# Optimization experiments

Hardware: AMD Instinct MI355X
Metric: run time of the kernel (lower is better)

Reference implementation:

```python
import jax, jax.numpy as jnp
import numpy as np

D = 1024
H = 16
DH = D // H
SCALE = DH ** -0.5
EPS = 1e-5


def setup_inputs() -> dict:
    key = jax.random.key(0)
    ks = jax.random.split(key, 8)
    B, K = 256, 64
    hidden = jax.random.normal(ks[0], (B, K, D), dtype=jnp.float32)
    active_mask = jax.random.bernoulli(ks[1], 0.5, (B, K))
    w = lambda k: jax.random.normal(k, (D, D), dtype=jnp.float32) * 0.02
    return {
        "hidden": hidden,
        "active_mask": active_mask,
        "W_q": w(ks[2]),
        "W_k": w(ks[3]),
        "W_v": w(ks[4]),
        "W_o": w(ks[5]),
        "ln_gamma": jnp.ones((D,), dtype=jnp.float32),
        "ln_beta": jnp.zeros((D,), dtype=jnp.float32),
    }


def reference(hidden, active_mask, W_q, W_k, W_v, W_o, ln_gamma, ln_beta):
    B, K, _ = hidden.shape
    # Linear (no bias): x @ W.T, then split heads -> [B, H, K, Dh]
    def heads(t):
        return t.reshape(B, K, H, DH).transpose(0, 2, 1, 3)
    Q = heads(hidden @ W_q.T)
    Km = heads(hidden @ W_k.T)
    V = heads(hidden @ W_v.T)
    # scaled dot-product scores [B, H, K, K]
    attn = jnp.einsum("bhqd,bhkd->bhqk", Q, Km) * SCALE
    attn = jax.nn.softmax(attn, axis=-1)
    # post-softmax row masking: inactive query rows get zero attention
    row_mask = active_mask[:, None, :, None].astype(attn.dtype)  # [B,1,K,1]
    attn = attn * row_mask
    out = jnp.einsum("bhqk,bhkd->bhqd", attn, V)
    out = out.transpose(0, 2, 1, 3).reshape(B, K, D)
    out = out @ W_o.T
    # gated residual: residual attention output only on active modules
    active_f = active_mask[:, :, None].astype(hidden.dtype)
    h_final = hidden + active_f * out
    # LayerNorm over last dim
    mu = jnp.mean(h_final, axis=-1, keepdims=True)
    var = jnp.var(h_final, axis=-1, keepdims=True)
    h_norm = (h_final - mu) * jax.lax.rsqrt(var + EPS)
    return h_norm * ln_gamma + ln_beta
```

## Files before the change

### kernel.cpp

```cpp
#include <hip/hip_runtime.h>
#include <hip/hip_bf16.h>
#include <stdint.h>

#define D_DIM 1024
#define NH 16
#define DHD 64
#define SEQ 64
#define NBATCH 256
#define M_TOT 16384
#define ATT_SCALE 0.125f
#define LN_EPS 1e-5f

#define BM 256
#define BN 256
#define BKT 64
#define NTK (D_DIM / BKT)

typedef __attribute__((ext_vector_type(8))) short bf16x8;
typedef __attribute__((ext_vector_type(4))) float f32x4;

__device__ __forceinline__ float bf2f(short s) {
  union { uint32_t u; float f; } c;
  c.u = ((uint32_t)(uint16_t)s) << 16;
  return c.f;
}

__device__ __forceinline__ short f2bf(float f) {
  union { __hip_bfloat16 h; short s; } c; c.h = __float2bfloat16(f);
  return c.s;
}

__device__ __forceinline__ bf16x8 cvt8(float4 a, float4 b) {
  bf16x8 r;
  r[0] = f2bf(a.x); r[1] = f2bf(a.y); r[2] = f2bf(a.z); r[3] = f2bf(a.w);
  r[4] = f2bf(b.x); r[5] = f2bf(b.y); r[6] = f2bf(b.z); r[7] = f2bf(b.w);
  return r;
}

__device__ __forceinline__ void cp16(const void* g, void* l) {
  __builtin_amdgcn_global_load_lds(
      (const __attribute__((address_space(1))) uint32_t*)g,
      (__attribute__((address_space(3))) uint32_t*)l, 16, 0, 0);
}

__global__ void conv_all(const float* __restrict__ Wq, const float* __restrict__ Wk,
                         const float* __restrict__ Wv, const float* __restrict__ Wo,
                         const float* __restrict__ H,
                         __hip_bfloat16* __restrict__ Wall,
                         __hip_bfloat16* __restrict__ Hb) {
  const size_t idx8 = ((size_t)blockIdx.x * 256 + threadIdx.x) * 8;
  const size_t WE = (size_t)4 * D_DIM * D_DIM;
  const float* src;
  __hip_bfloat16* dst;
  if (idx8 < WE) {
    int z = (int)(idx8 >> 20);
    size_t off = idx8 & ((1u << 20) - 1);
    src = ((z == 0) ? Wq : (z == 1) ? Wk : (z == 2) ? Wv : Wo) + off;
    dst = Wall + idx8;
  } else {
    size_t off = idx8 - WE;
    src = H + off;
    dst = Hb + off;
  }
  float4 a = ((const float4*)src)[0];
  float4 b = ((const float4*)src)[1];
  *(bf16x8*)(short*)dst = cvt8(a, b);
}

#define GEMM_TILE(J, CUR, NXT) do {                                           \
    _Pragma("unroll") for (int i_ = 0; i_ < 4; ++i_) {                        \
      af[i_][0] = *(const bf16x8*)(LdsA[CUR] + aoff + i_ * 2048 + colsw0);    \
      af[i_][1] = *(const bf16x8*)(LdsA[CUR] + aoff + i_ * 2048 + colsw1);    \
    }                                                                         \
    _Pragma("unroll") for (int q_ = 0; q_ < 2; ++q_) {                        \
      bfr[q_][0] = *(const bf16x8*)(LdsB[CUR] + boff + q_ * 2048 + colsw0);   \
      bfr[q_][1] = *(const bf16x8*)(LdsB[CUR] + boff + q_ * 2048 + colsw1);   \
    }                                                                         \
    __builtin_amdgcn_s_barrier();                                             \
    __asm volatile("s_waitcnt lgkmcnt(0)" ::: "memory");                      \
    __builtin_amdgcn_s_setprio(1);                                            \
    _Pragma("unroll") for (int i_ = 0; i_ < 4; ++i_)                          \
      _Pragma("unroll") for (int q_ = 0; q_ < 2; ++q_) {                      \
        acc[i_][q_] = __builtin_amdgcn_mfma_f32_16x16x32_bf16(                \
            af[i_][0], bfr[q_][0], acc[i_][q_], 0, 0, 0);                     \
        acc[i_][q_] = __builtin_amdgcn_mfma_f32_16x16x32_bf16(                \
            af[i_][1], bfr[q_][1], acc[i_][q_], 0, 0, 0);                     \
      }                                                                       \
    __builtin_amdgcn_s_setprio(0);                                            \
    __builtin_amdgcn_s_barrier();                                             \
    _Pragma("unroll") for (int q_ = 0; q_ < 2; ++q_) {                        \
      bfr[2 + q_][0] =                                                        \
          *(const bf16x8*)(LdsB[CUR] + boff + (2 + q_) * 2048 + colsw0);      \
      bfr[2 + q_][1] =                                                        \
          *(const bf16x8*)(LdsB[CUR] + boff + (2 + q_) * 2048 + colsw1);      \
    }                                                                         \
    if ((J) + 2 < NTK) { STG_A(CUR, (J) + 2, 0); STG_A(CUR, (J) + 2, 2); }    \
    __builtin_amdgcn_s_barrier();                                             \
    __asm volatile("s_waitcnt lgkmcnt(0)" ::: "memory");                      \
    __builtin_amdgcn_s_setprio(1);                                            \
    _Pragma("unroll") for (int i_ = 0; i_ < 4; ++i_)                          \
      _Pragma("unroll") for (int q_ = 0; q_ < 2; ++q_) {                      \
        acc[i_][2 + q_] = __builtin_amdgcn_mfma_f32_16x16x32_bf16(            \
            af[i_][0], bfr[2 + q_][0], acc[i_][2 + q_], 0, 0, 0);             \
        acc[i_][2 + q_] = __builtin_amdgcn_mfma_f32_16x16x32_bf16(            \
            af[i_][1], bfr[2 + q_][1], acc[i_][2 + q_], 0, 0, 0);             \
      }                                                                       \
    __builtin_amdgcn_s_setprio(0);                                            \
    __builtin_amdgcn_s_barrier();                                             \
    _Pragma("unroll") for (int i_ = 0; i_ < 4; ++i_) {                        \
      af[i_][0] =                                                             \
          *(const bf16x8*)(LdsA[CUR] + aoff + 8192 + i_ * 2048 + colsw0);     \
      af[i_][1] =                                                             \
          *(const bf16x8*)(LdsA[CUR] + aoff + 8192 + i_ * 2048 + colsw1);     \
    }                                                                         \
    if ((J) + 2 < NTK) {                                                      \
      STG_B(CUR, (J) + 2, 0); STG_B(CUR, (J) + 2, 1);                         \
      STG_B(CUR, (J) + 2, 2); STG_B(CUR, (J) + 2, 3);                         \
    }                                                                         \
    __builtin_amdgcn_s_barrier();                                             \
    __asm volatile("s_waitcnt lgkmcnt(0)" ::: "memory");                      \
    __builtin_amdgcn_s_setprio(1);                                            \
    _Pragma("unroll") for (int i_ = 0; i_ < 4; ++i_)                          \
      _Pragma("unroll") for (int q_ = 0; q_ < 2; ++q_) {                      \
        acc[4 + i_][2 + q_] = __builtin_amdgcn_mfma_f32_16x16x32_bf16(        \
            af[i_][0], bfr[2 + q_][0], acc[4 + i_][2 + q_], 0, 0, 0);         \
        acc[4 + i_][2 + q_] = __builtin_amdgcn_mfma_f32_16x16x32_bf16(        \
            af[i_][1], bfr[2 + q_][1], acc[4 + i_][2 + q_], 0, 0, 0);         \
      }                                                                       \
    __builtin_amdgcn_s_setprio(0);                                            \
    __builtin_amdgcn_s_barrier();                                             \
    if ((J) + 2 < NTK) { STG_A(CUR, (J) + 2, 1); STG_A(CUR, (J) + 2, 3); }    \
    __builtin_amdgcn_s_setprio(1);                                            \
    _Pragma("unroll") for (int i_ = 0; i_ < 4; ++i_)                          \
      _Pragma("unroll") for (int q_ = 0; q_ < 2; ++q_) {                      \
        acc[4 + i_][q_] = __builtin_amdgcn_mfma_f32_16x16x32_bf16(            \
            af[i_][0], bfr[q_][0], acc[4 + i_][q_], 0, 0, 0);                 \
        acc[4 + i_][q_] = __builtin_amdgcn_mfma_f32_16x16x32_bf16(            \
            af[i_][1], bfr[q_][1], acc[4 + i_][q_], 0, 0, 0);                 \
      }                                                                       \
    __builtin_amdgcn_s_setprio(0);                                            \
    if ((J) + 2 < NTK) {                                                      \
      __asm volatile("s_waitcnt vmcnt(8)" ::: "memory");                      \
    } else if ((J) + 1 < NTK) {                                               \
      __asm volatile("s_waitcnt vmcnt(0)" ::: "memory");                      \
    }                                                                         \
    __builtin_amdgcn_s_barrier();                                             \
  } while (0)

#define GEMM_PIPELINE() do {                                                  \
    STG_A(0, 0, 0); STG_A(0, 0, 1); STG_A(0, 0, 2); STG_A(0, 0, 3);           \
    STG_B(0, 0, 0); STG_B(0, 0, 1); STG_B(0, 0, 2); STG_B(0, 0, 3);           \
    STG_A(1, 1, 0); STG_A(1, 1, 1); STG_A(1, 1, 2); STG_A(1, 1, 3);           \
    STG_B(1, 1, 0); STG_B(1, 1, 1); STG_B(1, 1, 2); STG_B(1, 1, 3);           \
    __asm volatile("s_waitcnt vmcnt(8)" ::: "memory");                        \
    __builtin_amdgcn_s_barrier();                                             \
    _Pragma("unroll 1") for (int it_ = 0; it_ < NTK / 2; ++it_) {             \
      GEMM_TILE(2 * it_, 0, 1);                                               \
      GEMM_TILE(2 * it_ + 1, 1, 0);                                           \
    }                                                                         \
  } while (0)

__global__ void __launch_bounds__(512, 2)
gemm_qkv_bf(const __hip_bfloat16* __restrict__ Hb,
            const __hip_bfloat16* __restrict__ Wall,
            __hip_bfloat16* __restrict__ Qw,
            __hip_bfloat16* __restrict__ Kw,
            __hip_bfloat16* __restrict__ Vtw) {
  __shared__ __align__(16) char LdsA[2][BM * BKT * 2];
  __shared__ __align__(16) char LdsB[2][BN * BKT * 2];
  const int tid = threadIdx.x;
  const int lane = tid & 63, wave = tid >> 6;
  const int l16 = lane & 15, kq = lane >> 4;
  const int wr = wave >> 2, wc = wave & 3;
  const int m0 = blockIdx.x * BM, n0 = blockIdx.y * BN;
  const __hip_bfloat16* Bm = Wall + (size_t)blockIdx.z * D_DIM * D_DIM;
  const int wub = wave * 1024;
  const int srow = tid >> 3;
  const int scol8 = (((tid >> 3) & 7) ^ (tid & 7)) << 3;
  const size_t a_thr = (size_t)(m0 + srow) * D_DIM + scol8;
  const size_t b_thr = (size_t)(n0 + srow) * D_DIM + scol8;
  const int colsw0 = (kq * 16) ^ ((l16 & 7) << 4);
  const int colsw1 = (64 + kq * 16) ^ ((l16 & 7) << 4);
  const int aoff = (wr * 128 + l16) * 128;
  const int boff = (wc * 64 + l16) * 128;

  f32x4 acc[8][4] = {};
  bf16x8 af[4][2], bfr[4][2];

#define STG_A(BUF, JT, Q)                                                      \
  cp16(Hb + a_thr + (size_t)(Q) * (64 * D_DIM) + (JT) * BKT,                   \
       LdsA[BUF] + (Q) * 8192 + wub)
#define STG_B(BUF, JT, Q)                                                      \
  cp16(Bm + b_thr + (size_t)(Q) * (64 * D_DIM) + (JT) * BKT,                   \
       LdsB[BUF] + (Q) * 8192 + wub)

  GEMM_PIPELINE();

#undef STG_A
#undef STG_B

  __hip_bfloat16* outp = (blockIdx.z == 0) ? Qw : (blockIdx.z == 1) ? Kw : Vtw;
  const int zlt2 = (blockIdx.z < 2);
#pragma unroll
  for (int i = 0; i < 8; ++i) {
#pragma unroll
    for (int r = 0; r < 4; ++r) {
      int gm = m0 + wr * 128 + i * 16 + kq * 4 + r;
      int b = gm >> 6, ks = gm & 63;
#pragma unroll
      for (int jf = 0; jf < 4; ++jf) {
        int gn = n0 + wc * 64 + jf * 16 + l16;
        int h = gn >> 6, dh = gn & 63;
        size_t idx = zlt2 ? ((size_t)(b * NH + h) * SEQ + ks) * DHD + dh
                          : ((size_t)(b * NH + h) * DHD + dh) * SEQ + ks;
        outp[idx] = __float2bfloat16(acc[i][jf][r]);
      }
    }
  }
}

__global__ void attn_v2(__hip_bfloat16* Qw,
                        const __hip_bfloat16* __restrict__ Kw,
                        const __hip_bfloat16* __restrict__ Vtw,
                        const int* __restrict__ mask) {
  __shared__ __align__(16) __hip_bfloat16 Ps[4][16 * 72];
  const int tid = threadIdx.x;
  const int lane = tid & 63;
  const int wave = tid >> 6;
  const int l16 = lane & 15, kq = lane >> 4;
  const int hh = blockIdx.x * 4 + wave;
  const int b = hh >> 4;
  const size_t base = (size_t)hh * 4096;
  __hip_bfloat16* Pw = &Ps[wave][0];

  bf16x8 kf[2][4], vf[2][4], qf[4][2];
#pragma unroll
  for (int kk2 = 0; kk2 < 2; ++kk2)
#pragma unroll
    for (int j = 0; j < 4; ++j) {
      kf[kk2][j] = *(const bf16x8*)(Kw + base + (j * 16 + l16) * 64 + kk2 * 32 + kq * 8);
      vf[kk2][j] = *(const bf16x8*)(Vtw + base + (j * 16 + l16) * 64 + kk2 * 32 + kq * 8);
    }
#pragma unroll
  for (int qt = 0; qt < 4; ++qt)
#pragma unroll
    for (int kk2 = 0; kk2 < 2; ++kk2)
      qf[qt][kk2] = *(const bf16x8*)(Qw + base + (qt * 16 + l16) * 64 + kk2 * 32 + kq * 8);

#pragma unroll
  for (int qt = 0; qt < 4; ++qt) {
    f32x4 accS[4] = {};
#pragma unroll
    for (int kk2 = 0; kk2 < 2; ++kk2)
#pragma unroll
      for (int j = 0; j < 4; ++j)
        accS[j] = __builtin_amdgcn_mfma_f32_16x16x32_bf16(qf[qt][kk2], kf[kk2][j],
                                                          accS[j], 0, 0, 0);
#pragma unroll
    for (int r = 0; r < 4; ++r) {
      float sv[4];
      float m = -1e30f;
#pragma unroll
      for (int j = 0; j < 4; ++j) { sv[j] = accS[j][r] * ATT_SCALE; m = fmaxf(m, sv[j]); }
#pragma unroll
      for (int off = 1; off < 16; off <<= 1) m = fmaxf(m, __shfl_xor(m, off, 64));
      float s = 0.f;
#pragma unroll
      for (int j = 0; j < 4; ++j) { sv[j] = __expf(sv[j] - m); s += sv[j]; }
#pragma unroll
      for (int off = 1; off < 16; off <<= 1) s += __shfl_xor(s, off, 64);
      float inv = 1.0f / s;
      int ql = kq * 4 + r;
#pragma unroll
      for (int j = 0; j < 4; ++j)
        Pw[ql * 72 + j * 16 + l16] = __float2bfloat16(sv[j] * inv);
    }
    __asm volatile("s_waitcnt lgkmcnt(0)" ::: "memory");

    f32x4 accO[4] = {};
#pragma unroll
    for (int kk2 = 0; kk2 < 2; ++kk2) {
      bf16x8 a = *(const bf16x8*)((const short*)Pw + l16 * 72 + kk2 * 32 + kq * 8);
#pragma unroll
      for (int j = 0; j < 4; ++j)
        accO[j] = __builtin_amdgcn_mfma_f32_16x16x32_bf16(a, vf[kk2][j], accO[j], 0, 0, 0);
    }
    __asm volatile("s_waitcnt lgkmcnt(0)" ::: "memory");

#pragma unroll
    for (int r = 0; r < 4; ++r) {
      int q = qt * 16 + kq * 4 + r;
      float mk = mask[b * SEQ + q] ? 1.0f : 0.0f;
#pragma unroll
      for (int j = 0; j < 4; ++j)
        Qw[base + q * DHD + j * 16 + l16] = __float2bfloat16(accO[j][r] * mk);
    }
  }
}

__global__ void __launch_bounds__(512, 2)
gemm_o(const __hip_bfloat16* __restrict__ Ow,
       const __hip_bfloat16* __restrict__ WoB,
       const int* __restrict__ mask,
       __hip_bfloat16* Hb) {
  __shared__ __align__(16) char LdsA[2][BM * BKT * 2];
  __shared__ __align__(16) char LdsB[2][BN * BKT * 2];
  const int tid = threadIdx.x;
  const int lane = tid & 63, wave = tid >> 6;
  const int l16 = lane & 15, kq = lane >> 4;
  const int wr = wave >> 2, wc = wave & 3;
  const int m0 = blockIdx.x * BM, n0 = blockIdx.y * BN;
  const int wub = wave * 1024;
  const int srow = tid >> 3;
  const int scol8 = (((tid >> 3) & 7) ^ (tid & 7)) << 3;
  const size_t ao_thr = ((size_t)(m0 >> 6) << 16) + (srow << 6) + scol8;
  const size_t b_thr = (size_t)(n0 + srow) * D_DIM + scol8;
  const int colsw0 = (kq * 16) ^ ((l16 & 7) << 4);
  const int colsw1 = (64 + kq * 16) ^ ((l16 & 7) << 4);
  const int aoff = (wr * 128 + l16) * 128;
  const int boff = (wc * 64 + l16) * 128;

  f32x4 acc[8][4] = {};
  bf16x8 af[4][2], bfr[4][2];

#define STG_A(BUF, JT, Q)                                                      \
  cp16(Ow + ao_thr + ((size_t)(Q) << 16) + ((size_t)(JT) << 12),               \
       LdsA[BUF] + (Q) * 8192 + wub)
#define STG_B(BUF, JT, Q)                                                      \
  cp16(WoB + b_thr + (size_t)(Q) * (64 * D_DIM) + (JT) * BKT,                  \
       LdsB[BUF] + (Q) * 8192 + wub)

  GEMM_PIPELINE();

#undef STG_A
#undef STG_B

#pragma unroll
  for (int i = 0; i < 8; ++i) {
#pragma unroll
    for (int r = 0; r < 4; ++r) {
      int gm = m0 + wr * 128 + i * 16 + kq * 4 + r;
      float mk = mask[gm] ? 1.0f : 0.0f;
#pragma unroll
      for (int jf = 0; jf < 4; ++jf) {
        int gn = n0 + wc * 64 + jf * 16 + l16;
        size_t idx = (size_t)gm * D_DIM + gn;
        Hb[idx] = __float2bfloat16(__bfloat162float(Hb[idx]) + mk * acc[i][jf][r]);
      }
    }
  }
}

__global__ void __launch_bounds__(512)
ln_bf(const __hip_bfloat16* __restrict__ Hf,
      const float* __restrict__ gamma,
      const float* __restrict__ beta,
      float* __restrict__ out) {
  const int tid = threadIdx.x;
  const int wave = tid >> 6, lane = tid & 63;
  const int row = blockIdx.x * 8 + wave;
  const size_t rb = (size_t)row * D_DIM + lane * 16;

  bf16x8 v0 = *(const bf16x8*)((const short*)Hf + rb);
  bf16x8 v1 = *(const bf16x8*)((const short*)Hf + rb + 8);
  float f[16], s = 0.f, ss = 0.f;
#pragma unroll
  for (int k = 0; k < 8; ++k) { f[k] = bf2f(v0[k]); f[8 + k] = bf2f(v1[k]); }
#pragma unroll
  for (int k = 0; k < 16; ++k) { s += f[k]; ss += f[k] * f[k]; }
#pragma unroll
  for (int off = 1; off < 64; off <<= 1) {
    s += __shfl_xor(s, off, 64);
    ss += __shfl_xor(ss, off, 64);
  }
  const float mu = s * (1.0f / D_DIM);
  const float var = ss * (1.0f / D_DIM) - mu * mu;
  const float rs = rsqrtf(var + LN_EPS);

  const float4* gp = (const float4*)(gamma + lane * 16);
  const float4* bp = (const float4*)(beta + lane * 16);
  float4* op = (float4*)(out + rb);
#pragma unroll
  for (int q = 0; q < 4; ++q) {
    float4 g = gp[q], bb = bp[q];
    float4 o;
    o.x = (f[q * 4 + 0] - mu) * rs * g.x + bb.x;
    o.y = (f[q * 4 + 1] - mu) * rs * g.y + bb.y;
    o.z = (f[q * 4 + 2] - mu) * rs * g.z + bb.z;
    o.w = (f[q * 4 + 3] - mu) * rs * g.w + bb.w;
    op[q] = o;
  }
}

extern "C" void kernel_launch(void* const* d_in, const int* in_sizes, int n_in,
                              void* d_out, int out_size, void* d_ws, size_t ws_size,
                              hipStream_t stream) {
  const float* hidden = (const float*)d_in[0];
  const int* mask = (const int*)d_in[1];
  const float* Wq = (const float*)d_in[2];
  const float* Wk = (const float*)d_in[3];
  const float* Wv = (const float*)d_in[4];
  const float* Wo = (const float*)d_in[5];
  const float* gamma = (const float*)d_in[6];
  const float* beta = (const float*)d_in[7];
  float* out = (float*)d_out;

  const size_t SZ = (size_t)M_TOT * D_DIM;
  __hip_bfloat16* Hb   = (__hip_bfloat16*)d_ws;
  __hip_bfloat16* Kw   = Hb + SZ;
  __hip_bfloat16* Qw   = Hb + 2 * SZ;
  __hip_bfloat16* Vtw  = Hb + 3 * SZ;
  __hip_bfloat16* Wall = Hb + 4 * SZ;

  conv_all<<<dim3(10240), 256, 0, stream>>>(Wq, Wk, Wv, Wo, hidden, Wall, Hb);
  gemm_qkv_bf<<<dim3(64, 4, 3), 512, 0, stream>>>(Hb, Wall, Qw, Kw, Vtw);
  attn_v2<<<dim3(1024), 256, 0, stream>>>(Qw, Kw, Vtw, mask);
  gemm_o<<<dim3(64, 4), 512, 0, stream>>>(Qw, Wall + 3 * D_DIM * D_DIM, mask, Hb);
  ln_bf<<<dim3(2048), 512, 0, stream>>>(Hb, gamma, beta, out);
}
```

Before: 341.8 us.

## Shrink GEMM tiles to 128x128 with 4 waves and simplified pipeline

Both projection GEMMs move from 256x256 tiles with 8 waves to 128x128 tiles with 4 waves. The interleaved multi-phase MFMA/staging schedule becomes a single load-all-fragments-then-compute step per K tile. The aim is more blocks for better CU occupancy and load balance, since the old grids had only 256 or 768 blocks. In exchange, each block reuses loaded data less, global and LDS traffic per FLOP rises, and the loads no longer overlap the MFMAs within a tile.

Result: slower. 363.6 us (+6.4%).

```diff
diff --git a/kernel.cpp b/kernel.cpp
--- a/kernel.cpp
+++ b/kernel.cpp
@@ -11,8 +11,8 @@
 #define ATT_SCALE 0.125f
 #define LN_EPS 1e-5f
 
-#define BM 256
-#define BN 256
+#define BMS 128
+#define BNS 128
 #define BKT 64
 #define NTK (D_DIM / BKT)
 
@@ -67,79 +67,32 @@
   *(bf16x8*)(short*)dst = cvt8(a, b);
 }
 
-#define GEMM_TILE(J, CUR, NXT) do {                                           \
+#define GEMM_TILE_S(J, CUR, NXT) do {                                         \
     _Pragma("unroll") for (int i_ = 0; i_ < 4; ++i_) {                        \
       af[i_][0] = *(const bf16x8*)(LdsA[CUR] + aoff + i_ * 2048 + colsw0);    \
       af[i_][1] = *(const bf16x8*)(LdsA[CUR] + aoff + i_ * 2048 + colsw1);    \
     }                                                                         \
-    _Pragma("unroll") for (int q_ = 0; q_ < 2; ++q_) {                        \
-      bfr[q_][0] = *(const bf16x8*)(LdsB[CUR] + boff + q_ * 2048 + colsw0);   \
-      bfr[q_][1] = *(const bf16x8*)(LdsB[CUR] + boff + q_ * 2048 + colsw1);   \
+    _Pragma("unroll") for (int j_ = 0; j_ < 4; ++j_) {                        \
+      bfr[j_][0] = *(const bf16x8*)(LdsB[CUR] + boff + j_ * 2048 + colsw0);   \
+      bfr[j_][1] = *(const bf16x8*)(LdsB[CUR] + boff + j_ * 2048 + colsw1);   \
     }                                                                         \
-    __builtin_amdgcn_s_barrier();                                             \
-    __asm volatile("s_waitcnt lgkmcnt(0)" ::: "memory");                      \
     __builtin_amdgcn_s_setprio(1);                                            \
     _Pragma("unroll") for (int i_ = 0; i_ < 4; ++i_)                          \
-      _Pragma("unroll") for (int q_ = 0; q_ < 2; ++q_) {                      \
-        acc[i_][q_] = __builtin_amdgcn_mfma_f32_16x16x32_bf16(                \
-            af[i_][0], bfr[q_][0], acc[i_][q_], 0, 0, 0);                     \
-        acc[i_][q_] = __builtin_amdgcn_mfma_f32_16x16x32_bf16(                \
-            af[i_][1], bfr[q_][1], acc[i_][q_], 0, 0, 0);                     \
+      _Pragma("unroll") for (int j_ = 0; j_ < 4; ++j_) {                      \
+        acc[i_][j_] = __builtin_amdgcn_mfma_f32_16x16x32_bf16(                \
+            af[i_][0], bfr[j_][0], acc[i_][j_], 0, 0, 0);                     \
+        acc[i_][j_] = __builtin_amdgcn_mfma_f32_16x16x32_bf16(                \
+            af[i_][1], bfr[j_][1], acc[i_][j_], 0, 0, 0);                     \
       }                                                                       \
     __builtin_amdgcn_s_setprio(0);                                            \
+    __asm volatile("s_waitcnt lgkmcnt(0)" ::: "memory");                      \
+    __builtin_amdgcn_sched_barrier(0);                                        \
     __builtin_amdgcn_s_barrier();                                             \
-    _Pragma("unroll") for (int q_ = 0; q_ < 2; ++q_) {                        \
-      bfr[2 + q_][0] =                                                        \
-          *(const bf16x8*)(LdsB[CUR] + boff + (2 + q_) * 2048 + colsw0);      \
-      bfr[2 + q_][1] =                                                        \
-          *(const bf16x8*)(LdsB[CUR] + boff + (2 + q_) * 2048 + colsw1);      \
-    }                                                                         \
-    if ((J) + 2 < NTK) { STG_A(CUR, (J) + 2, 0); STG_A(CUR, (J) + 2, 2); }    \
-    __builtin_amdgcn_s_barrier();                                             \
-    __asm volatile("s_waitcnt lgkmcnt(0)" ::: "memory");                      \
-    __builtin_amdgcn_s_setprio(1);                                            \
-    _Pragma("unroll") for (int i_ = 0; i_ < 4; ++i_)                          \
-      _Pragma("unroll") for (int q_ = 0; q_ < 2; ++q_) {                      \
-        acc[i_][2 + q_] = __builtin_amdgcn_mfma_f32_16x16x32_bf16(            \
-            af[i_][0], bfr[2 + q_][0], acc[i_][2 + q_], 0, 0, 0);             \
-        acc[i_][2 + q_] = __builtin_amdgcn_mfma_f32_16x16x32_bf16(            \
-            af[i_][1], bfr[2 + q_][1], acc[i_][2 + q_], 0, 0, 0);             \
-      }                                                                       \
-    __builtin_amdgcn_s_setprio(0);                                            \
-    __builtin_amdgcn_s_barrier();                                             \
-    _Pragma("unroll") for (int i_ = 0; i_ < 4; ++i_) {                        \
-      af[i_][0] =                                                             \
-          *(const bf16x8*)(LdsA[CUR] + aoff + 8192 + i_ * 2048 + colsw0);     \
-      af[i_][1] =                                                             \
-          *(const bf16x8*)(LdsA[CUR] + aoff + 8192 + i_ * 2048 + colsw1);     \
-    }                                                                         \
     if ((J) + 2 < NTK) {                                                      \
+      STG_A(CUR, (J) + 2, 0); STG_A(CUR, (J) + 2, 1);                         \
+      STG_A(CUR, (J) + 2, 2); STG_A(CUR, (J) + 2, 3);                         \
       STG_B(CUR, (J) + 2, 0); STG_B(CUR, (J) + 2, 1);                         \
       STG_B(CUR, (J) + 2, 2); STG_B(CUR, (J) + 2, 3);                         \
-    }                                                                         \
-    __builtin_amdgcn_s_barrier();                                             \
-    __asm volatile("s_waitcnt lgkmcnt(0)" ::: "memory");                      \
-    __builtin_amdgcn_s_setprio(1);                                            \
-    _Pragma("unroll") for (int i_ = 0; i_ < 4; ++i_)                          \
-      _Pragma("unroll") for (int q_ = 0; q_ < 2; ++q_) {                      \
-        acc[4 + i_][2 + q_] = __builtin_amdgcn_mfma_f32_16x16x32_bf16(        \
-            af[i_][0], bfr[2 + q_][0], acc[4 + i_][2 + q_], 0, 0, 0);         \
-        acc[4 + i_][2 + q_] = __builtin_amdgcn_mfma_f32_16x16x32_bf16(        \
-            af[i_][1], bfr[2 + q_][1], acc[4 + i_][2 + q_], 0, 0, 0);         \
-      }                                                                       \
-    __builtin_amdgcn_s_setprio(0);                                            \
-    __builtin_amdgcn_s_barrier();                                             \
-    if ((J) + 2 < NTK) { STG_A(CUR, (J) + 2, 1); STG_A(CUR, (J) + 2, 3); }    \
-    __builtin_amdgcn_s_setprio(1);                                            \
-    _Pragma("unroll") for (int i_ = 0; i_ < 4; ++i_)                          \
-      _Pragma("unroll") for (int q_ = 0; q_ < 2; ++q_) {                      \
-        acc[4 + i_][q_] = __builtin_amdgcn_mfma_f32_16x16x32_bf16(            \
-            af[i_][0], bfr[q_][0], acc[4 + i_][q_], 0, 0, 0);                 \
-        acc[4 + i_][q_] = __builtin_amdgcn_mfma_f32_16x16x32_bf16(            \
-            af[i_][1], bfr[q_][1], acc[4 + i_][q_], 0, 0, 0);                 \
-      }                                                                       \
-    __builtin_amdgcn_s_setprio(0);                                            \
-    if ((J) + 2 < NTK) {                                                      \
       __asm volatile("s_waitcnt vmcnt(8)" ::: "memory");                      \
     } else if ((J) + 1 < NTK) {                                               \
       __asm volatile("s_waitcnt vmcnt(0)" ::: "memory");                      \
@@ -147,7 +100,7 @@
     __builtin_amdgcn_s_barrier();                                             \
   } while (0)
 
-#define GEMM_PIPELINE() do {                                                  \
+#define GEMM_PIPELINE_S() do {                                                \
     STG_A(0, 0, 0); STG_A(0, 0, 1); STG_A(0, 0, 2); STG_A(0, 0, 3);           \
     STG_B(0, 0, 0); STG_B(0, 0, 1); STG_B(0, 0, 2); STG_B(0, 0, 3);           \
     STG_A(1, 1, 0); STG_A(1, 1, 1); STG_A(1, 1, 2); STG_A(1, 1, 3);           \
@@ -155,24 +108,24 @@
     __asm volatile("s_waitcnt vmcnt(8)" ::: "memory");                        \
     __builtin_amdgcn_s_barrier();                                             \
     _Pragma("unroll 1") for (int it_ = 0; it_ < NTK / 2; ++it_) {             \
-      GEMM_TILE(2 * it_, 0, 1);                                               \
-      GEMM_TILE(2 * it_ + 1, 1, 0);                                           \
+      GEMM_TILE_S(2 * it_, 0, 1);                                             \
+      GEMM_TILE_S(2 * it_ + 1, 1, 0);                                         \
     }                                                                         \
   } while (0)
 
-__global__ void __launch_bounds__(512, 2)
+__global__ void __launch_bounds__(256, 2)
 gemm_qkv_bf(const __hip_bfloat16* __restrict__ Hb,
             const __hip_bfloat16* __restrict__ Wall,
             __hip_bfloat16* __restrict__ Qw,
             __hip_bfloat16* __restrict__ Kw,
             __hip_bfloat16* __restrict__ Vtw) {
-  __shared__ __align__(16) char LdsA[2][BM * BKT * 2];
-  __shared__ __align__(16) char LdsB[2][BN * BKT * 2];
+  __shared__ __align__(16) char LdsA[2][BMS * BKT * 2];
+  __shared__ __align__(16) char LdsB[2][BNS * BKT * 2];
   const int tid = threadIdx.x;
   const int lane = tid & 63, wave = tid >> 6;
   const int l16 = lane & 15, kq = lane >> 4;
-  const int wr = wave >> 2, wc = wave & 3;
-  const int m0 = blockIdx.x * BM, n0 = blockIdx.y * BN;
+  const int wr = wave >> 1, wc = wave & 1;
+  const int m0 = blockIdx.x * BMS, n0 = blockIdx.y * BNS;
   const __hip_bfloat16* Bm = Wall + (size_t)blockIdx.z * D_DIM * D_DIM;
   const int wub = wave * 1024;
   const int srow = tid >> 3;
@@ -181,20 +134,20 @@
   const size_t b_thr = (size_t)(n0 + srow) * D_DIM + scol8;
   const int colsw0 = (kq * 16) ^ ((l16 & 7) << 4);
   const int colsw1 = (64 + kq * 16) ^ ((l16 & 7) << 4);
-  const int aoff = (wr * 128 + l16) * 128;
+  const int aoff = (wr * 64 + l16) * 128;
   const int boff = (wc * 64 + l16) * 128;
 
-  f32x4 acc[8][4] = {};
+  f32x4 acc[4][4] = {};
   bf16x8 af[4][2], bfr[4][2];
 
 #define STG_A(BUF, JT, Q)                                                      \
-  cp16(Hb + a_thr + (size_t)(Q) * (64 * D_DIM) + (JT) * BKT,                   \
-       LdsA[BUF] + (Q) * 8192 + wub)
+  cp16(Hb + a_thr + (size_t)(Q) * (32 * D_DIM) + (JT) * BKT,                   \
+       LdsA[BUF] + (Q) * 4096 + wub)
 #define STG_B(BUF, JT, Q)                                                      \
-  cp16(Bm + b_thr + (size_t)(Q) * (64 * D_DIM) + (JT) * BKT,                   \
-       LdsB[BUF] + (Q) * 8192 + wub)
-
-  GEMM_PIPELINE();
+  cp16(Bm + b_thr + (size_t)(Q) * (32 * D_DIM) + (JT) * BKT,                   \
+       LdsB[BUF] + (Q) * 4096 + wub)
+
+  GEMM_PIPELINE_S();
 
 #undef STG_A
 #undef STG_B
@@ -202,10 +155,10 @@
   __hip_bfloat16* outp = (blockIdx.z == 0) ? Qw : (blockIdx.z == 1) ? Kw : Vtw;
   const int zlt2 = (blockIdx.z < 2);
 #pragma unroll
-  for (int i = 0; i < 8; ++i) {
+  for (int i = 0; i < 4; ++i) {
 #pragma unroll
     for (int r = 0; r < 4; ++r) {
-      int gm = m0 + wr * 128 + i * 16 + kq * 4 + r;
+      int gm = m0 + wr * 64 + i * 16 + kq * 4 + r;
       int b = gm >> 6, ks = gm & 63;
 #pragma unroll
       for (int jf = 0; jf < 4; ++jf) {
@@ -298,18 +251,18 @@
   }
 }
 
-__global__ void __launch_bounds__(512, 2)
+__global__ void __launch_bounds__(256, 2)
 gemm_o(const __hip_bfloat16* __restrict__ Ow,
        const __hip_bfloat16* __restrict__ WoB,
        const int* __restrict__ mask,
        __hip_bfloat16* Hb) {
-  __shared__ __align__(16) char LdsA[2][BM * BKT * 2];
-  __shared__ __align__(16) char LdsB[2][BN * BKT * 2];
+  __shared__ __align__(16) char LdsA[2][BMS * BKT * 2];
+  __shared__ __align__(16) char LdsB[2][BNS * BKT * 2];
   const int tid = threadIdx.x;
   const int lane = tid & 63, wave = tid >> 6;
   const int l16 = lane & 15, kq = lane >> 4;
-  const int wr = wave >> 2, wc = wave & 3;
-  const int m0 = blockIdx.x * BM, n0 = blockIdx.y * BN;
+  const int wr = wave >> 1, wc = wave & 1;
+  const int m0 = blockIdx.x * BMS, n0 = blockIdx.y * BNS;
   const int wub = wave * 1024;
   const int srow = tid >> 3;
   const int scol8 = (((tid >> 3) & 7) ^ (tid & 7)) << 3;
@@ -317,29 +270,30 @@
   const size_t b_thr = (size_t)(n0 + srow) * D_DIM + scol8;
   const int colsw0 = (kq * 16) ^ ((l16 & 7) << 4);
   const int colsw1 = (64 + kq * 16) ^ ((l16 & 7) << 4);
-  const int aoff = (wr * 128 + l16) * 128;
+  const int aoff = (wr * 64 + l16) * 128;
   const int boff = (wc * 64 + l16) * 128;
 
-  f32x4 acc[8][4] = {};
+  f32x4 acc[4][4] = {};
   bf16x8 af[4][2], bfr[4][2];
 
 #define STG_A(BUF, JT, Q)                                                      \
-  cp16(Ow + ao_thr + ((size_t)(Q) << 16) + ((size_t)(JT) << 12),               \
-       LdsA[BUF] + (Q) * 8192 + wub)
+  cp16(Ow + ao_thr + ((size_t)((Q) >> 1) << 16) + (((Q) & 1) << 11) +          \
+           ((size_t)(JT) << 12),                                               \
+       LdsA[BUF] + (Q) * 4096 + wub)
 #define STG_B(BUF, JT, Q)                                                      \
-  cp16(WoB + b_thr + (size_t)(Q) * (64 * D_DIM) + (JT) * BKT,                  \
-       LdsB[BUF] + (Q) * 8192 + wub)
-
-  GEMM_PIPELINE();
+  cp16(WoB + b_thr + (size_t)(Q) * (32 * D_DIM) + (JT) * BKT,                  \
+       LdsB[BUF] + (Q) * 4096 + wub)
+
+  GEMM_PIPELINE_S();
 
 #undef STG_A
 #undef STG_B
 
 #pragma unroll
-  for (int i = 0; i < 8; ++i) {
+  for (int i = 0; i < 4; ++i) {
 #pragma unroll
     for (int r = 0; r < 4; ++r) {
-      int gm = m0 + wr * 128 + i * 16 + kq * 4 + r;
+      int gm = m0 + wr * 64 + i * 16 + kq * 4 + r;
       float mk = mask[gm] ? 1.0f : 0.0f;
 #pragma unroll
       for (int jf = 0; jf < 4; ++jf) {
@@ -413,8 +367,8 @@
   __hip_bfloat16* Wall = Hb + 4 * SZ;
 
   conv_all<<<dim3(10240), 256, 0, stream>>>(Wq, Wk, Wv, Wo, hidden, Wall, Hb);
-  gemm_qkv_bf<<<dim3(64, 4, 3), 512, 0, stream>>>(Hb, Wall, Qw, Kw, Vtw);
+  gemm_qkv_bf<<<dim3(128, 8, 3), 256, 0, stream>>>(Hb, Wall, Qw, Kw, Vtw);
   attn_v2<<<dim3(1024), 256, 0, stream>>>(Qw, Kw, Vtw, mask);
-  gemm_o<<<dim3(64, 4), 512, 0, stream>>>(Qw, Wall + 3 * D_DIM * D_DIM, mask, Hb);
+  gemm_o<<<dim3(128, 8), 256, 0, stream>>>(Qw, Wall + 3 * D_DIM * D_DIM, mask, Hb);
   ln_bf<<<dim3(2048), 512, 0, stream>>>(Hb, gamma, beta, out);
 }
```
